# Kernel tuning notes

Measured on AMD Instinct MI355X. Metric: run time of the kernel, lower is better.

## Reference

```python
import jax, jax.numpy as jnp
import numpy as np


def _conv(x, w, stride, padding):
    # x: [N, Cin, H, W], w: [Cout, Cin, kh, kw]
    return jax.lax.conv_general_dilated(
        x, w, window_strides=(stride, stride), padding=padding,
        dimension_numbers=("NCHW", "OIHW", "NCHW"))


def _reflect_pad1(x):
    return jnp.pad(x, ((0, 0), (0, 0), (1, 1), (1, 1)), mode="reflect")


def setup_inputs() -> dict:
    key = jax.random.key(0)
    k1, k2, k3, k4 = jax.random.split(key, 4)
    B, C, H, W = 16, 3, 512, 512
    NC = 20  # num_channels (intermediate width)
    # xavier-uniform-like scales
    x = jax.random.normal(k1, (B, C, H, W), dtype=jnp.float32)
    w1 = jax.random.normal(k2, (NC, 1, 4, 4), dtype=jnp.float32) * (6.0 / (1 * 16 + NC * 16)) ** 0.5
    w2 = jax.random.normal(k3, (NC, NC, 4, 4), dtype=jnp.float32) * (6.0 / (NC * 16 + NC * 16)) ** 0.5
    w3 = jax.random.normal(k4, (1, NC, 3, 3), dtype=jnp.float32) * (6.0 / (NC * 9 + 1 * 9)) ** 0.5
    return {"x": x, "w1": w1, "w2": w2, "w3": w3}


def reference(x, w1, w2, w3):
    # Original torch code loops over input channels; equivalently fold the
    # channel dim into the batch dim and run the whole pipeline once.
    B, C, H, W = x.shape
    xr = x.reshape(B * C, 1, H, W)
    # stage 1: reflect pad 1 + 4x4 stride-2 conv + relu
    o1 = jax.nn.relu(_conv(_reflect_pad1(xr), w1, 2, "VALID"))  # [B*C, NC, 256, 256]
    # stage 2: reflect pad 1 + 4x4 stride-2 conv + relu
    o2 = jax.nn.relu(_conv(_reflect_pad1(o1), w2, 2, "VALID"))  # [B*C, NC, 128, 128]
    # stage 3: 3x3 conv, zero padding 1, + relu -> 1 channel per input channel
    o3 = jax.nn.relu(_conv(o2, w3, 1, ((1, 1), (1, 1))))        # [B*C, 1, 128, 128]
    Ho, Wo = o3.shape[-2], o3.shape[-1]
    return o3.reshape(B, C, Ho, Wo)
```

## Files before the change

kernel.cpp:

```cpp
#include <hip/hip_runtime.h>


#define NC 20
#define TS 12
#define AR 16
#define SO1 48
#define PS1 770
#define SO2 16
#define PS2 226

#define W2F_OFF 256
#define W3_OFF  5376
#define WP_N    5556

typedef _Float16 h2  __attribute__((ext_vector_type(2)));
typedef __fp16   hq2 __attribute__((ext_vector_type(2)));
typedef _Float16 h8  __attribute__((ext_vector_type(8)));
typedef float    f32x16 __attribute__((ext_vector_type(16)));

__device__ __forceinline__ float dot2(unsigned int a, unsigned int b, float c) {
    return __builtin_amdgcn_fdot2(__builtin_bit_cast(h2, a),
                                  __builtin_bit_cast(h2, b), c, false);
}
__device__ __forceinline__ unsigned int packh(float a, float b) {
    _Float16 ha = (_Float16)a, hb = (_Float16)b;
    return (unsigned int)__builtin_bit_cast(unsigned short, ha) |
           ((unsigned int)__builtin_bit_cast(unsigned short, hb) << 16);
}
__device__ __forceinline__ unsigned int pkrtz(float a, float b) {
    hq2 r = __builtin_amdgcn_cvt_pkrtz(a, b);
    return __builtin_bit_cast(unsigned int, r);
}
__device__ __forceinline__ unsigned short f2h(float a) {
    _Float16 h = (_Float16)a;
    return __builtin_bit_cast(unsigned short, h);
}
__device__ __forceinline__ int refl256(int q) {
    q = (q < 0) ? -q : q; return (q > 255) ? 510 - q : q;
}
__device__ __forceinline__ int refl512(int q) {
    q = (q < 0) ? -q : q; return (q > 511) ? 1022 - q : q;
}

__global__ __launch_bounds__(256) void pack_weights(
    const float* __restrict__ w1, const float* __restrict__ w2,
    const float* __restrict__ w3, unsigned int* __restrict__ wp)
{
    const int i = blockIdx.x * 256 + threadIdx.x;
    if (i >= WP_N) return;
    if (i < W2F_OFF) {
        const int lane = i >> 2, jp = i & 3;
        const int ch = lane & 31, k0 = (lane >> 5) * 8 + 2 * jp;
        wp[i] = (ch < NC) ? packh(w1[ch * 16 + k0], w1[ch * 16 + k0 + 1]) : 0u;
    } else if (i < W3_OFF) {
        const int t = i - W2F_OFF;
        const int cin = t >> 8, r = t & 255;
        const int lane = r >> 2, jp = r & 3;
        const int cout = lane & 31, k0 = (lane >> 5) * 8 + 2 * jp;
        wp[i] = (cout < NC) ? packh(w2[(cout * NC + cin) * 16 + k0],
                                    w2[(cout * NC + cin) * 16 + k0 + 1]) : 0u;
    } else {
        const int t = i - W3_OFF;
        const int c = t / 9;
        const int r = t - c * 9;
        const int di = r / 3, wh = r - di * 3;
        const float* row = w3 + c * 9 + di * 3;
        float a, b;
        if (wh == 0)      { a = row[0]; b = row[1]; }
        else if (wh == 1) { a = row[2]; b = 0.f;    }
        else              { a = 0.f;    b = row[2]; }
        wp[i] = packh(a, b);
    }
}

__device__ __forceinline__ void load_taps(
    const float* __restrict__ xi, int t0, int h, int wv, int kh,
    bool rowEdge, bool colEdge, int vb, int v0, int v1, int v2, int v3,
    unsigned int xw[4][4])
{
    #pragma unroll
    for (int i = 0; i < 4; ++i) {
        const int c = wv + 4 * i;
        const int t = t0 + 14 * h + c;
        int rlo, rhi;
        if (!rowEdge) {
            rlo = 2 * t - 3 + 2 * kh;
            rhi = rlo + 1;
        } else {
            const int mr = refl256(t - 1);
            const int rb = 2 * mr - 1 + 2 * kh;
            rlo = refl512(rb);
            rhi = refl512(rb + 1);
        }
        const float* __restrict__ plo = xi + rlo * 512;
        const float* __restrict__ phi = xi + rhi * 512;
        float f0, f1, f2, f3, f4, f5, f6, f7;
        if (!colEdge) {
            f0 = plo[vb]; f1 = plo[vb + 1]; f2 = plo[vb + 2]; f3 = plo[vb + 3];
            f4 = phi[vb]; f5 = phi[vb + 1]; f6 = phi[vb + 2]; f7 = phi[vb + 3];
        } else {
            f0 = plo[v0]; f1 = plo[v1]; f2 = plo[v2]; f3 = plo[v3];
            f4 = phi[v0]; f5 = phi[v1]; f6 = phi[v2]; f7 = phi[v3];
        }
        xw[i][0] = pkrtz(f0, f1); xw[i][1] = pkrtz(f2, f3);
        xw[i][2] = pkrtz(f4, f5); xw[i][3] = pkrtz(f6, f7);
    }
}

__global__ __launch_bounds__(256, 4) void ds_fused(
    const float* __restrict__ x,
    const unsigned int* __restrict__ wp,
    float* __restrict__ out)
{
    __shared__ __attribute__((aligned(16))) unsigned short s_o1[NC * PS1];
    __shared__ __attribute__((aligned(16))) unsigned short s_o2[NC * PS2];

    const int bid  = blockIdx.x;
    const int img  = bid / 121;
    const int t121 = bid - img * 121;
    const int ty   = t121 / 11;
    const int tx   = t121 - ty * 11;
    const int y0   = ty * TS;
    const int x0   = tx * TS;
    const int tid  = threadIdx.x;
    const int lane = tid & 63;
    const int wv   = tid >> 6;
    const int l31  = lane & 31;
    const int kh   = lane >> 5;

    const float* __restrict__ xi = x + (size_t)img * (512 * 512);
    const uint4* __restrict__ w1f = (const uint4*)wp;
    const uint4* __restrict__ w2f = (const uint4*)(wp + W2F_OFF);
    const unsigned int* __restrict__ w3p = wp + W3_OFF;

    const int t0 = 2 * y0 - 2;
    const int s0 = 2 * x0 - 2;

    const int sA = s0 + l31;
    const bool rowEdge = (ty == 0) || (ty == 10);
    const bool colEdge = (tx == 0) || (tx == 10);
    const bool interior = !rowEdge && !colEdge;
    const int vb = 2 * sA - 3;
    int v0 = 0, v1 = 0, v2 = 0, v3 = 0;
    if (colEdge) {
        const int n2 = refl256(sA - 1);
        const int vbb = 2 * n2 - 1;
        v0 = refl512(vbb);     v1 = refl512(vbb + 1);
        v2 = refl512(vbb + 2); v3 = refl512(vbb + 3);
    }
    const h8 w1frag = __builtin_bit_cast(h8, w1f[lane]);

    const int q  = 32 * wv + l31;
    const int qc = (q < 98) ? q : 0;
    const int li = (qc * 2341) >> 15;
    const int jl = qc - li * 14;
    const int offA = (2 * li + 2 * kh) * SO1 + 2 * jl;

    unsigned int xw0[4][4];
    load_taps(xi, t0, 0, wv, kh, rowEdge, colEdge, vb, v0, v1, v2, v3, xw0);

    #pragma unroll
    for (int i = 0; i < 4; ++i) {
        const int c = wv + 4 * i;
        uint4 aw; aw.x = xw0[i][0]; aw.y = xw0[i][1];
                  aw.z = xw0[i][2]; aw.w = xw0[i][3];
        f32x16 o = {};
        o = __builtin_amdgcn_mfma_f32_32x32x16_f16(
                __builtin_bit_cast(h8, aw), w1frag, o, 0, 0, 0);
        if (l31 < NC) {
            unsigned int* wr = (unsigned int*)&s_o1[l31 * PS1 + c * SO1 + 4 * kh];
            wr[0]  = pkrtz(fmaxf(o[0],  0.f), fmaxf(o[1],  0.f));
            wr[1]  = pkrtz(fmaxf(o[2],  0.f), fmaxf(o[3],  0.f));
            wr[4]  = pkrtz(fmaxf(o[4],  0.f), fmaxf(o[5],  0.f));
            wr[5]  = pkrtz(fmaxf(o[6],  0.f), fmaxf(o[7],  0.f));
            wr[8]  = pkrtz(fmaxf(o[8],  0.f), fmaxf(o[9],  0.f));
            wr[9]  = pkrtz(fmaxf(o[10], 0.f), fmaxf(o[11], 0.f));
            wr[12] = pkrtz(fmaxf(o[12], 0.f), fmaxf(o[13], 0.f));
            wr[13] = pkrtz(fmaxf(o[14], 0.f), fmaxf(o[15], 0.f));
        }
    }

    unsigned int xw1[4][4];
    load_taps(xi, t0, 1, wv, kh, rowEdge, colEdge, vb, v0, v1, v2, v3, xw1);

    #pragma unroll
    for (int h = 0; h < 2; ++h) {
        if (h == 1) {
            __syncthreads();
            #pragma unroll
            for (int i = 0; i < 4; ++i) {
                const int c = wv + 4 * i;
                uint4 aw; aw.x = xw1[i][0]; aw.y = xw1[i][1];
                          aw.z = xw1[i][2]; aw.w = xw1[i][3];
                f32x16 o = {};
                o = __builtin_amdgcn_mfma_f32_32x32x16_f16(
                        __builtin_bit_cast(h8, aw), w1frag, o, 0, 0, 0);
                if (l31 < NC) {
                    unsigned int* wr =
                        (unsigned int*)&s_o1[l31 * PS1 + c * SO1 + 4 * kh];
                    wr[0]  = pkrtz(fmaxf(o[0],  0.f), fmaxf(o[1],  0.f));
                    wr[1]  = pkrtz(fmaxf(o[2],  0.f), fmaxf(o[3],  0.f));
                    wr[4]  = pkrtz(fmaxf(o[4],  0.f), fmaxf(o[5],  0.f));
                    wr[5]  = pkrtz(fmaxf(o[6],  0.f), fmaxf(o[7],  0.f));
                    wr[8]  = pkrtz(fmaxf(o[8],  0.f), fmaxf(o[9],  0.f));
                    wr[9]  = pkrtz(fmaxf(o[10], 0.f), fmaxf(o[11], 0.f));
                    wr[12] = pkrtz(fmaxf(o[12], 0.f), fmaxf(o[13], 0.f));
                    wr[13] = pkrtz(fmaxf(o[14], 0.f), fmaxf(o[15], 0.f));
                }
            }
        }
        __syncthreads();

        f32x16 acc = {};
        #pragma unroll
        for (int cin = 0; cin < NC; ++cin) {
            const uint4 bw = w2f[cin * 64 + lane];
            const unsigned short* pA = &s_o1[cin * PS1 + offA];
            uint4 aw;
            aw.x = *(const unsigned int*)(pA);
            aw.y = *(const unsigned int*)(pA + 2);
            aw.z = *(const unsigned int*)(pA + SO1);
            aw.w = *(const unsigned int*)(pA + SO1 + 2);
            acc = __builtin_amdgcn_mfma_f32_32x32x16_f16(
                      __builtin_bit_cast(h8, aw),
                      __builtin_bit_cast(h8, bw), acc, 0, 0, 0);
        }

        if (l31 < NC) {
            #pragma unroll
            for (int p = 0; p < 16; ++p) {
                const int mr = (p & 3) + 8 * (p >> 2) + 4 * kh;
                const int qq = 32 * wv + mr;
                if (qq < 98) {
                    const int li2 = (qq * 2341) >> 15;
                    const int jl2 = qq - li2 * 14;
                    const int ilt = 7 * h + li2;
                    if (interior) {
                        s_o2[l31 * PS2 + ilt * SO2 + jl2] = f2h(fmaxf(acc[p], 0.f));
                    } else {
                        const int oi = y0 - 1 + ilt, oj = x0 - 1 + jl2;
                        const bool val = (oi >= 0) && (oi < 128) &&
                                         (oj >= 0) && (oj < 128);
                        s_o2[l31 * PS2 + ilt * SO2 + jl2] =
                            val ? f2h(fmaxf(acc[p], 0.f)) : (unsigned short)0;
                    }
                }
            }
        }
    }
    __syncthreads();

    if (tid < TS * TS) {
        const int oy = tid / TS;
        const int ox = tid - oy * TS;
        const int e  = ox & ~1;
        const int par = ox & 1;
        float accc = 0.f;
        for (int c = 0; c < NC; ++c) {
            #pragma unroll
            for (int di = 0; di < 3; ++di) {
                const unsigned int* row =
                    (const unsigned int*)&s_o2[c * PS2 + (oy + di) * SO2 + e];
                const unsigned int d0 = row[0];
                const unsigned int d1 = row[1];
                const unsigned int mm = __builtin_amdgcn_perm(d1, d0, 0x05040302u);
                const unsigned int u0 = par ? mm : d0;
                const unsigned int wa = w3p[c * 9 + di * 3 + 0];
                const unsigned int wb = w3p[c * 9 + di * 3 + 1];
                const unsigned int wc = w3p[c * 9 + di * 3 + 2];
                accc = dot2(u0, wa, accc);
                accc = dot2(d1, par ? wc : wb, accc);
            }
        }
        const int gy = y0 + oy, gx = x0 + ox;
        if (gy < 128 && gx < 128)
            out[(size_t)img * (128 * 128) + gy * 128 + gx] = fmaxf(accc, 0.f);
    }
}

extern "C" void kernel_launch(void* const* d_in, const int* in_sizes, int n_in,
                              void* d_out, int out_size, void* d_ws, size_t ws_size,
                              hipStream_t stream) {
    const float* x  = (const float*)d_in[0];
    const float* w1 = (const float*)d_in[1];
    const float* w2 = (const float*)d_in[2];
    const float* w3 = (const float*)d_in[3];
    unsigned int* wp = (unsigned int*)d_ws;
    float* out = (float*)d_out;
    pack_weights<<<dim3((WP_N + 255) / 256), dim3(256), 0, stream>>>(w1, w2, w3, wp);
    ds_fused<<<dim3(48 * 121), dim3(256), 0, stream>>>(x, wp, out);
}
```

Measured before the change: 168.3 us.

## Split stage-1 channels into two groups to shrink LDS and raise occupancy

Stage-1 output is now kept in LDS for only 10 of the 20 channels at a time. The kernel alternates stage-1 MFMA and stage-2 accumulation over the two channel groups, which roughly halves the s_o1 footprint, and launch bounds are raised to 5 blocks per CU. The s_o2 row stride is also tightened from 16 to 14 columns (PS2 226→198) so its index is linear and the interior epilogue skips the div/mod. In exchange, stage-1 MFMAs are recomputed for each group, with half of the lanes' outputs discarded each time, and extra __syncthreads barriers are added.

```diff
diff --git a/kernel.cpp b/kernel.cpp
--- a/kernel.cpp
+++ b/kernel.cpp
@@ -2,12 +2,11 @@
 
 
 #define NC 20
+#define CG 10
 #define TS 12
-#define AR 16
 #define SO1 48
 #define PS1 770
-#define SO2 16
-#define PS2 226
+#define PS2 198
 
 #define W2F_OFF 256
 #define W3_OFF  5376
@@ -107,12 +106,87 @@
     }
 }
 
-__global__ __launch_bounds__(256, 4) void ds_fused(
+__device__ __forceinline__ void stage_a(
+    const unsigned int xw[4][4], h8 w1frag,
+    unsigned short* __restrict__ s_o1, int g, int wv, int l31, int kh)
+{
+    const int cl = l31 - CG * g;
+    const bool wr_en = (cl >= 0) && (cl < CG);
+    #pragma unroll
+    for (int i = 0; i < 4; ++i) {
+        const int c = wv + 4 * i;
+        uint4 aw; aw.x = xw[i][0]; aw.y = xw[i][1];
+                  aw.z = xw[i][2]; aw.w = xw[i][3];
+        f32x16 o = {};
+        o = __builtin_amdgcn_mfma_f32_32x32x16_f16(
+                __builtin_bit_cast(h8, aw), w1frag, o, 0, 0, 0);
+        if (wr_en) {
+            unsigned int* wr = (unsigned int*)&s_o1[cl * PS1 + c * SO1 + 4 * kh];
+            wr[0]  = pkrtz(fmaxf(o[0],  0.f), fmaxf(o[1],  0.f));
+            wr[1]  = pkrtz(fmaxf(o[2],  0.f), fmaxf(o[3],  0.f));
+            wr[4]  = pkrtz(fmaxf(o[4],  0.f), fmaxf(o[5],  0.f));
+            wr[5]  = pkrtz(fmaxf(o[6],  0.f), fmaxf(o[7],  0.f));
+            wr[8]  = pkrtz(fmaxf(o[8],  0.f), fmaxf(o[9],  0.f));
+            wr[9]  = pkrtz(fmaxf(o[10], 0.f), fmaxf(o[11], 0.f));
+            wr[12] = pkrtz(fmaxf(o[12], 0.f), fmaxf(o[13], 0.f));
+            wr[13] = pkrtz(fmaxf(o[14], 0.f), fmaxf(o[15], 0.f));
+        }
+    }
+}
+
+__device__ __forceinline__ void stage_b(
+    f32x16& acc, const unsigned short* __restrict__ s_o1,
+    const uint4* __restrict__ w2f, int g, int offA, int lane)
+{
+    #pragma unroll
+    for (int ci = 0; ci < CG; ++ci) {
+        const int cin = CG * g + ci;
+        const uint4 bw = w2f[cin * 64 + lane];
+        const unsigned short* pA = &s_o1[ci * PS1 + offA];
+        uint4 aw;
+        aw.x = *(const unsigned int*)(pA);
+        aw.y = *(const unsigned int*)(pA + 2);
+        aw.z = *(const unsigned int*)(pA + SO1);
+        aw.w = *(const unsigned int*)(pA + SO1 + 2);
+        acc = __builtin_amdgcn_mfma_f32_32x32x16_f16(
+                  __builtin_bit_cast(h8, aw),
+                  __builtin_bit_cast(h8, bw), acc, 0, 0, 0);
+    }
+}
+
+__device__ __forceinline__ void epilogue(
+    const f32x16& acc, unsigned short* __restrict__ s_o2,
+    int h, int wv, int l31, int kh, bool interior, int y0, int x0)
+{
+    if (l31 < NC) {
+        unsigned short* base = &s_o2[l31 * PS2 + 98 * h];
+        #pragma unroll
+        for (int p = 0; p < 16; ++p) {
+            const int mr = (p & 3) + 8 * (p >> 2) + 4 * kh;
+            const int qq = 32 * wv + mr;
+            if (qq < 98) {
+                if (interior) {
+                    base[qq] = f2h(fmaxf(acc[p], 0.f));
+                } else {
+                    const int li2 = (qq * 2341) >> 15;
+                    const int jl2 = qq - li2 * 14;
+                    const int oi = y0 - 1 + 7 * h + li2;
+                    const int oj = x0 - 1 + jl2;
+                    const bool val = (oi >= 0) && (oi < 128) &&
+                                     (oj >= 0) && (oj < 128);
+                    base[qq] = val ? f2h(fmaxf(acc[p], 0.f)) : (unsigned short)0;
+                }
+            }
+        }
+    }
+}
+
+__global__ __launch_bounds__(256, 5) void ds_fused(
     const float* __restrict__ x,
     const unsigned int* __restrict__ wp,
     float* __restrict__ out)
 {
-    __shared__ __attribute__((aligned(16))) unsigned short s_o1[NC * PS1];
+    __shared__ __attribute__((aligned(16))) unsigned short s_o1[CG * PS1];
     __shared__ __attribute__((aligned(16))) unsigned short s_o2[NC * PS2];
 
     const int bid  = blockIdx.x;
@@ -159,108 +233,50 @@
     unsigned int xw0[4][4];
     load_taps(xi, t0, 0, wv, kh, rowEdge, colEdge, vb, v0, v1, v2, v3, xw0);
 
-    #pragma unroll
-    for (int i = 0; i < 4; ++i) {
-        const int c = wv + 4 * i;
-        uint4 aw; aw.x = xw0[i][0]; aw.y = xw0[i][1];
-                  aw.z = xw0[i][2]; aw.w = xw0[i][3];
-        f32x16 o = {};
-        o = __builtin_amdgcn_mfma_f32_32x32x16_f16(
-                __builtin_bit_cast(h8, aw), w1frag, o, 0, 0, 0);
-        if (l31 < NC) {
-            unsigned int* wr = (unsigned int*)&s_o1[l31 * PS1 + c * SO1 + 4 * kh];
-            wr[0]  = pkrtz(fmaxf(o[0],  0.f), fmaxf(o[1],  0.f));
-            wr[1]  = pkrtz(fmaxf(o[2],  0.f), fmaxf(o[3],  0.f));
-            wr[4]  = pkrtz(fmaxf(o[4],  0.f), fmaxf(o[5],  0.f));
-            wr[5]  = pkrtz(fmaxf(o[6],  0.f), fmaxf(o[7],  0.f));
-            wr[8]  = pkrtz(fmaxf(o[8],  0.f), fmaxf(o[9],  0.f));
-            wr[9]  = pkrtz(fmaxf(o[10], 0.f), fmaxf(o[11], 0.f));
-            wr[12] = pkrtz(fmaxf(o[12], 0.f), fmaxf(o[13], 0.f));
-            wr[13] = pkrtz(fmaxf(o[14], 0.f), fmaxf(o[15], 0.f));
-        }
-    }
+    stage_a(xw0, w1frag, s_o1, 0, wv, l31, kh);
+    __syncthreads();
 
     unsigned int xw1[4][4];
     load_taps(xi, t0, 1, wv, kh, rowEdge, colEdge, vb, v0, v1, v2, v3, xw1);
 
-    #pragma unroll
-    for (int h = 0; h < 2; ++h) {
-        if (h == 1) {
-            __syncthreads();
-            #pragma unroll
-            for (int i = 0; i < 4; ++i) {
-                const int c = wv + 4 * i;
-                uint4 aw; aw.x = xw1[i][0]; aw.y = xw1[i][1];
-                          aw.z = xw1[i][2]; aw.w = xw1[i][3];
-                f32x16 o = {};
-                o = __builtin_amdgcn_mfma_f32_32x32x16_f16(
-                        __builtin_bit_cast(h8, aw), w1frag, o, 0, 0, 0);
-                if (l31 < NC) {
-                    unsigned int* wr =
-                        (unsigned int*)&s_o1[l31 * PS1 + c * SO1 + 4 * kh];
-                    wr[0]  = pkrtz(fmaxf(o[0],  0.f), fmaxf(o[1],  0.f));
-                    wr[1]  = pkrtz(fmaxf(o[2],  0.f), fmaxf(o[3],  0.f));
-                    wr[4]  = pkrtz(fmaxf(o[4],  0.f), fmaxf(o[5],  0.f));
-                    wr[5]  = pkrtz(fmaxf(o[6],  0.f), fmaxf(o[7],  0.f));
-                    wr[8]  = pkrtz(fmaxf(o[8],  0.f), fmaxf(o[9],  0.f));
-                    wr[9]  = pkrtz(fmaxf(o[10], 0.f), fmaxf(o[11], 0.f));
-                    wr[12] = pkrtz(fmaxf(o[12], 0.f), fmaxf(o[13], 0.f));
-                    wr[13] = pkrtz(fmaxf(o[14], 0.f), fmaxf(o[15], 0.f));
-                }
-            }
-        }
-        __syncthreads();
-
-        f32x16 acc = {};
-        #pragma unroll
-        for (int cin = 0; cin < NC; ++cin) {
-            const uint4 bw = w2f[cin * 64 + lane];
-            const unsigned short* pA = &s_o1[cin * PS1 + offA];
-            uint4 aw;
-            aw.x = *(const unsigned int*)(pA);
-            aw.y = *(const unsigned int*)(pA + 2);
-            aw.z = *(const unsigned int*)(pA + SO1);
-            aw.w = *(const unsigned int*)(pA + SO1 + 2);
-            acc = __builtin_amdgcn_mfma_f32_32x32x16_f16(
-                      __builtin_bit_cast(h8, aw),
-                      __builtin_bit_cast(h8, bw), acc, 0, 0, 0);
-        }
-
-        if (l31 < NC) {
-            #pragma unroll
-            for (int p = 0; p < 16; ++p) {
-                const int mr = (p & 3) + 8 * (p >> 2) + 4 * kh;
-                const int qq = 32 * wv + mr;
-                if (qq < 98) {
-                    const int li2 = (qq * 2341) >> 15;
-                    const int jl2 = qq - li2 * 14;
-                    const int ilt = 7 * h + li2;
-                    if (interior) {
-                        s_o2[l31 * PS2 + ilt * SO2 + jl2] = f2h(fmaxf(acc[p], 0.f));
-                    } else {
-                        const int oi = y0 - 1 + ilt, oj = x0 - 1 + jl2;
-                        const bool val = (oi >= 0) && (oi < 128) &&
-                                         (oj >= 0) && (oj < 128);
-                        s_o2[l31 * PS2 + ilt * SO2 + jl2] =
-                            val ? f2h(fmaxf(acc[p], 0.f)) : (unsigned short)0;
-                    }
-                }
-            }
-        }
-    }
+    f32x16 acc = {};
+    stage_b(acc, s_o1, w2f, 0, offA, lane);
+    __syncthreads();
+
+    stage_a(xw0, w1frag, s_o1, 1, wv, l31, kh);
+    __syncthreads();
+
+    stage_b(acc, s_o1, w2f, 1, offA, lane);
+    epilogue(acc, s_o2, 0, wv, l31, kh, interior, y0, x0);
+    __syncthreads();
+
+    stage_a(xw1, w1frag, s_o1, 0, wv, l31, kh);
+    __syncthreads();
+
+    f32x16 acc2 = {};
+    stage_b(acc2, s_o1, w2f, 0, offA, lane);
+    __syncthreads();
+
+    stage_a(xw1, w1frag, s_o1, 1, wv, l31, kh);
+    __syncthreads();
+
+    stage_b(acc2, s_o1, w2f, 1, offA, lane);
+    epilogue(acc2, s_o2, 1, wv, l31, kh, interior, y0, x0);
     __syncthreads();
 
     if (tid < TS * TS) {
         const int oy = tid / TS;
         const int ox = tid - oy * TS;
-        const int e  = ox & ~1;
         const int par = ox & 1;
+        const int e0  = ox & ~1;
         float accc = 0.f;
         for (int c = 0; c < NC; ++c) {
+            const unsigned short* plane = &s_o2[c * PS2];
             #pragma unroll
             for (int di = 0; di < 3; ++di) {
+                const int r = oy + di;
                 const unsigned int* row =
-                    (const unsigned int*)&s_o2[c * PS2 + (oy + di) * SO2 + e];
+                    (const unsigned int*)&plane[r * 14 + e0];
                 const unsigned int d0 = row[0];
                 const unsigned int d1 = row[1];
                 const unsigned int mm = __builtin_amdgcn_perm(d1, d0, 0x05040302u);
```

Result: slower. 283.8 us (+68.6%).
